# Performance work log

Measured on AMD Instinct MI355X. Metric: run time of the kernel, lower is better.

## Reference

```python
import jax, jax.numpy as jnp
import numpy as np
from jax import lax

K = 3  # kernel_size
PAD = K // 2

def setup_inputs() -> dict:
    key = jax.random.key(0)
    ks = jax.random.split(key, 8)
    B, C, H, W = 8, 96, 128, 128
    x = jax.random.normal(ks[0], (B, C, H, W), dtype=jnp.float32)
    s = 0.05
    dw_w = jax.random.normal(ks[1], (C, 1, 3, 3), dtype=jnp.float32) * s   # depthwise 3x3
    dw_b = jax.random.normal(ks[2], (C,), dtype=jnp.float32) * s
    pw1_w = jax.random.normal(ks[3], (C // 2, C), dtype=jnp.float32) * s   # 1x1: C -> C/2
    pw1_b = jax.random.normal(ks[4], (C // 2,), dtype=jnp.float32) * s
    pw2_w = jax.random.normal(ks[5], (K * K, C // 2), dtype=jnp.float32) * s  # 1x1: C/2 -> 9
    pw2_b = jax.random.normal(ks[6], (K * K,), dtype=jnp.float32) * s
    return {"x": x, "dw_w": dw_w, "dw_b": dw_b, "pw1_w": pw1_w,
            "pw1_b": pw1_b, "pw2_w": pw2_w, "pw2_b": pw2_b}

def _unfold3x3(x):
    # x: (B,C,H,W) -> patches (B,C,9,H,W), index order (di*3+dj) matching F.unfold
    B, C, H, W = x.shape
    xp = jnp.pad(x, ((0, 0), (0, 0), (PAD, PAD), (PAD, PAD)))
    return jnp.stack([xp[:, :, i:i + H, j:j + W] for i in range(K) for j in range(K)], axis=2)

def _forward(x, dw_w, dw_b, pw1_w, pw1_b, pw2_w, pw2_b):
    B, C, H, W = x.shape
    # kernel predictor: depthwise 3x3 -> 1x1 -> leaky_relu(0.2) -> 1x1
    h = lax.conv_general_dilated(x, dw_w, (1, 1), ((PAD, PAD), (PAD, PAD)),
                                 dimension_numbers=("NCHW", "OIHW", "NCHW"),
                                 feature_group_count=C)
    h = h + dw_b[None, :, None, None]
    h = jnp.einsum("bchw,oc->bohw", h, pw1_w) + pw1_b[None, :, None, None]
    h = jnp.where(h >= 0, h, 0.2 * h)  # LeakyReLU(0.2)
    kw = jnp.einsum("bchw,oc->bohw", h, pw2_w) + pw2_b[None, :, None, None]  # (B,9,H,W)
    kw = jax.nn.softmax(kw, axis=1)
    patches = _unfold3x3(x)                      # (B,C,9,H,W)
    x_smooth = jnp.einsum("bckhw,bkhw->bchw", patches, kw)
    return x_smooth

def reference(x, dw_w, dw_b, pw1_w, pw1_b, pw2_w, pw2_b):
    return _forward(x, dw_w, dw_b, pw1_w, pw1_b, pw2_w, pw2_b)
```

## Files before the change

kernel.cpp:

```cpp
#include <hip/hip_runtime.h>
#include <math.h>

#define Cc 96
#define Hh 128
#define Ww 128
#define HWsz (Hh*Ww)
#define TW 16
#define TH 8
#define LROW 18
#define LPLANE 180
#define CPAD 104

typedef _Float16 h2 __attribute__((ext_vector_type(2)));
typedef short    s8v __attribute__((ext_vector_type(8)));
typedef float    f4v __attribute__((ext_vector_type(4)));

__device__ __forceinline__ unsigned pkrtz_u(float a, float b) {
    return __builtin_bit_cast(unsigned, __builtin_amdgcn_cvt_pkrtz(a, b));
}
__device__ __forceinline__ h2 pk2(float a, float b) {
    return __builtin_bit_cast(h2, __builtin_amdgcn_cvt_pkrtz(a, b));
}
__device__ __forceinline__ h2 u2h(unsigned u) { return __builtin_bit_cast(h2, u); }
__device__ __forceinline__ unsigned cvt_pk_bf16(float lo, float hi) {
    unsigned r;
    asm("v_cvt_pk_bf16_f32 %0, %1, %2" : "=v"(r) : "v"(lo), "v"(hi));
    return r;
}

__host__ __device__ __forceinline__ unsigned f2bf(float f) {
    unsigned u = __float_as_uint(f);
    return (u + 0x7fffu + ((u >> 16) & 1u)) >> 16;
}

#define GETW(v, wi) ((wi)==0 ? (v).x : (wi)==1 ? (v).y : (wi)==2 ? (v).z : (v).w)

#define OFF_WDW 0
#define OFF_W2  480
#define OFF_P1B 704
#define OFF_A   768
#define NPK     3072
#define WLDS_N  752

__global__ void alpf_prep(const float* __restrict__ dw_w, const float* __restrict__ dw_b,
                          const float* __restrict__ pw1_w, const float* __restrict__ pw1_b,
                          const float* __restrict__ pw2_w, unsigned* __restrict__ wpk)
{
    int i = blockIdx.x * 256 + threadIdx.x;
    if (i >= NPK) return;
    unsigned v = 0u;
    if (i < OFF_W2) {
        int g = i / 120, rem = i % 120, ks = rem / 40, s = rem % 40;
        int chb = 32*ks + 8*g;
        if (s < 4) v = pkrtz_u(dw_b[chb + 2*s], dw_b[chb + 2*s + 1]);
        else { int t = (s - 4) / 4, d = (s - 4) % 4;
               v = pkrtz_u(dw_w[(chb + 2*d)*9 + t], dw_w[(chb + 2*d + 1)*9 + t]); }
    } else if (i < OFF_P1B) {
        int idx = i - OFF_W2; int g = idx / 56, s = idx % 56;
        if (s < 54) { int k = s / 6, mm = s % 6, m = mm / 2, rp = mm % 2;
            int o = 16*m + 4*g + 2*rp;
            v = pkrtz_u(pw2_w[k*48 + o], pw2_w[k*48 + o + 1]); }
    } else if (i < OFF_P1B + 48) {
        v = __float_as_uint(pw1_b[i - OFF_P1B]);
    } else if (i >= OFF_A) {
        int idx = i - OFF_A; int f = idx / 256, rem = idx % 256, l = rem / 4, d = rem % 4;
        int m = f / 3, ks = f % 3;
        int o  = 16*m + (l & 15);
        int ch = 32*ks + 8*(l >> 4) + 2*d;
        v = f2bf(pw1_w[o*Cc + ch]) | (f2bf(pw1_w[o*Cc + ch + 1]) << 16);
    }
    wpk[i] = v;
}

__global__ __launch_bounds__(256, 4)
void alpf_fused(const float* __restrict__ x,
                const float* __restrict__ pw2_b,
                const unsigned* __restrict__ wpk,
                float* __restrict__ out)
{
    __shared__ unsigned short lx[LPLANE * CPAD];
    __shared__ unsigned wlds[WLDS_N];

    const int tid = threadIdx.x;

    const int nwg   = gridDim.x;
    const int chunk = nwg >> 3;
    const int logical = (blockIdx.x & 7) * chunk + (blockIdx.x >> 3);
    const int tx = logical & 7;
    const int ty = (logical >> 3) & 15;
    const int b  = logical >> 7;
    const int x0 = tx * TW;
    const int y0 = ty * TH;
    const float* __restrict__ xb = x + (size_t)b * Cc * HWsz;

    if (tid < 188)
        *reinterpret_cast<uint4*>(&wlds[tid * 4]) =
            *reinterpret_cast<const uint4*>(wpk + tid * 4);

    const int lane = tid & 63;
    const int g    = lane >> 4;
    const int c15  = lane & 15;
    const int wv   = tid >> 6;

    s8v Af[9];
    #pragma unroll
    for (int f = 0; f < 9; ++f)
        Af[f] = __builtin_bit_cast(s8v,
            *reinterpret_cast<const uint4*>(wpk + OFF_A + (f*64 + lane)*4));

    for (int t = tid; t < 960; t += 256) {
        const int ri  = t / 96;
        const int rem = t - ri * 96;
        const int cp  = rem >> 1;
        const int ph  = rem & 1;
        const int gy  = y0 - 1 + ri;
        const bool okr = (gy >= 0) & (gy < Hh);
        const int gyc = okr ? gy : 0;
        const int chA = 2 * cp;
        const float* pA = xb + (size_t)chA * HWsz + gyc * Ww + x0 + 8 * ph;
        const float* pB = pA + HWsz;
        float4 a0 = *reinterpret_cast<const float4*>(pA);
        float4 a1 = *reinterpret_cast<const float4*>(pA + 4);
        float4 b0 = *reinterpret_cast<const float4*>(pB);
        float4 b1 = *reinterpret_cast<const float4*>(pB + 4);
        if (!okr) { a0 = make_float4(0,0,0,0); a1 = a0; b0 = a0; b1 = a0; }
        const int ecol  = ph ? (x0 + 16) : (x0 - 1);
        const bool oke  = okr & (ecol >= 0) & (ecol < Ww);
        const int ecolc = (ecol >= 0 && ecol < Ww) ? ecol : 0;
        const float* pE = xb + (size_t)chA * HWsz + gyc * Ww + ecolc;
        float ea = pE[0], eb = pE[HWsz];
        if (!oke) { ea = 0.f; eb = 0.f; }
        const int prow = ri * LROW + 1 + 8 * ph;
        #define STG(q, va, vb) \
            *reinterpret_cast<unsigned*>(&lx[(prow + (q)) * CPAD + chA]) = pkrtz_u(va, vb)
        STG(0, a0.x, b0.x); STG(1, a0.y, b0.y); STG(2, a0.z, b0.z); STG(3, a0.w, b0.w);
        STG(4, a1.x, b1.x); STG(5, a1.y, b1.y); STG(6, a1.z, b1.z); STG(7, a1.w, b1.w);
        #undef STG
        const int eq = ri * LROW + (ph ? 17 : 0);
        *reinterpret_cast<unsigned*>(&lx[eq * CPAD + chA]) = pkrtz_u(ea, eb);
    }
    __syncthreads();

    f4v acc[3][2];
    #pragma unroll
    for (int m = 0; m < 3; ++m) {
        const f4v bb = *reinterpret_cast<const f4v*>(&wlds[OFF_P1B + 16*m + 4*g]);
        acc[m][0] = bb;
        acc[m][1] = bb;
    }

    #pragma unroll
    for (int ks = 0; ks < 3; ++ks) {
        const int base = (g*3 + ks) * 40;
        const uint4 wb = *reinterpret_cast<const uint4*>(&wlds[base]);
        uint4 wt[9];
        #pragma unroll
        for (int t = 0; t < 9; ++t)
            wt[t] = *reinterpret_cast<const uint4*>(&wlds[base + 4 + 4*t]);
        uint4 xc_[4][3];
        #pragma unroll
        for (int r = 0; r < 4; ++r)
            #pragma unroll
            for (int d = 0; d < 3; ++d)
                xc_[r][d] = *reinterpret_cast<const uint4*>(
                    &lx[((2*wv + r)*LROW + c15 + d)*CPAD + 32*ks + 8*g]);
        #pragma unroll
        for (int n = 0; n < 2; ++n) {
            h2 b0 = u2h(wb.x), b1 = u2h(wb.y), b2 = u2h(wb.z), b3 = u2h(wb.w);
            #pragma unroll
            for (int t = 0; t < 9; ++t) {
                const int dy = t / 3, dx = t - 3*dy;
                const uint4 xv = xc_[n + dy][dx];
                b0 = __builtin_elementwise_fma(u2h(xv.x), u2h(wt[t].x), b0);
                b1 = __builtin_elementwise_fma(u2h(xv.y), u2h(wt[t].y), b1);
                b2 = __builtin_elementwise_fma(u2h(xv.z), u2h(wt[t].z), b2);
                b3 = __builtin_elementwise_fma(u2h(xv.w), u2h(wt[t].w), b3);
            }
            uint4 bq;
            bq.x = cvt_pk_bf16((float)b0.x, (float)b0.y);
            bq.y = cvt_pk_bf16((float)b1.x, (float)b1.y);
            bq.z = cvt_pk_bf16((float)b2.x, (float)b2.y);
            bq.w = cvt_pk_bf16((float)b3.x, (float)b3.y);
            const s8v Bf = __builtin_bit_cast(s8v, bq);
            acc[0][n] = __builtin_amdgcn_mfma_f32_16x16x32_bf16(Af[0 + ks], Bf, acc[0][n], 0, 0, 0);
            acc[1][n] = __builtin_amdgcn_mfma_f32_16x16x32_bf16(Af[3 + ks], Bf, acc[1][n], 0, 0, 0);
            acc[2][n] = __builtin_amdgcn_mfma_f32_16x16x32_bf16(Af[6 + ks], Bf, acc[2][n], 0, 0, 0);
        }
    }

    h2 tpk[2][3][2];
    #pragma unroll
    for (int n = 0; n < 2; ++n)
        #pragma unroll
        for (int m = 0; m < 3; ++m)
            #pragma unroll
            for (int rp = 0; rp < 2; ++rp) {
                float a = acc[m][n][2*rp], c = acc[m][n][2*rp + 1];
                a = (a >= 0.f) ? a : 0.2f * a;
                c = (c >= 0.f) ? c : 0.2f * c;
                tpk[n][m][rp] = pk2(a, c);
            }

    uint4 w2q[14];
    #pragma unroll
    for (int j = 0; j < 14; ++j)
        w2q[j] = *reinterpret_cast<const uint4*>(&wlds[OFF_W2 + g*56 + 4*j]);

    float kwr[2][9];
    #pragma unroll
    for (int k = 0; k < 9; ++k) {
        #pragma unroll
        for (int n = 0; n < 2; ++n) {
            h2 s = pk2(0.f, 0.f);
            #pragma unroll
            for (int m = 0; m < 3; ++m)
                #pragma unroll
                for (int rp = 0; rp < 2; ++rp) {
                    const int d = k*6 + 2*m + rp;
                    s = __builtin_elementwise_fma(tpk[n][m][rp],
                                                  u2h(GETW(w2q[d >> 2], d & 3)), s);
                }
            kwr[n][k] = (float)s.x + (float)s.y;
        }
    }
    #pragma unroll
    for (int n = 0; n < 2; ++n)
        #pragma unroll
        for (int k = 0; k < 9; ++k) {
            float v = kwr[n][k];
            v += __shfl_xor(v, 16);
            v += __shfl_xor(v, 32);
            kwr[n][k] = v + pw2_b[k];
        }

    const int nn  = (lane >> 4) & 1;
    const int chh = lane >> 5;
    const int row = 2*wv + nn;

    float kw[9];
    #pragma unroll
    for (int k = 0; k < 9; ++k) kw[k] = nn ? kwr[1][k] : kwr[0][k];

    float mx = kw[0];
    #pragma unroll
    for (int k = 1; k < 9; ++k) mx = fmaxf(mx, kw[k]);
    float sum = 0.f;
    #pragma unroll
    for (int k = 0; k < 9; ++k) { kw[k] = __expf(kw[k] - mx); sum += kw[k]; }
    const float inv = 1.f / sum;
    h2 kwp[9];
    #pragma unroll
    for (int k = 0; k < 9; ++k) { kw[k] *= inv; kwp[k] = pk2(kw[k], kw[k]); }

    const unsigned short* lb = &lx[(row * LROW + c15) * CPAD];
    float* __restrict__ ob = out + (size_t)b * Cc * HWsz + (size_t)(y0 + row) * Ww + (x0 + c15);
    #pragma unroll 2
    for (int cg = 0; cg < 6; ++cg) {
        const int c0 = chh * 48 + cg * 8;
        uint4 tp[9];
        #pragma unroll
        for (int k = 0; k < 9; ++k) {
            const int dy = k / 3, dx = k - 3 * dy;
            tp[k] = *reinterpret_cast<const uint4*>(&lb[(dy*LROW + dx)*CPAD + c0]);
        }
        #pragma unroll
        for (int l = 0; l < 4; ++l) {
            h2 a0 = u2h(GETW(tp[0], l)) * kwp[0];
            h2 a1 = u2h(GETW(tp[1], l)) * kwp[1];
            h2 a2 = u2h(GETW(tp[2], l)) * kwp[2];
            a0 = __builtin_elementwise_fma(u2h(GETW(tp[3], l)), kwp[3], a0);
            a1 = __builtin_elementwise_fma(u2h(GETW(tp[4], l)), kwp[4], a1);
            a2 = __builtin_elementwise_fma(u2h(GETW(tp[5], l)), kwp[5], a2);
            a0 = __builtin_elementwise_fma(u2h(GETW(tp[6], l)), kwp[6], a0);
            a1 = __builtin_elementwise_fma(u2h(GETW(tp[7], l)), kwp[7], a1);
            a2 = __builtin_elementwise_fma(u2h(GETW(tp[8], l)), kwp[8], a2);
            float olo = (float)a0.x + (float)a1.x + (float)a2.x;
            float ohi = (float)a0.y + (float)a1.y + (float)a2.y;
            ob[(size_t)(c0 + 2*l)     * HWsz] = olo;
            ob[(size_t)(c0 + 2*l + 1) * HWsz] = ohi;
        }
    }
}

extern "C" void kernel_launch(void* const* d_in, const int* in_sizes, int n_in,
                              void* d_out, int out_size, void* d_ws, size_t ws_size,
                              hipStream_t stream)
{
    const float* x     = (const float*)d_in[0];
    const float* dw_w  = (const float*)d_in[1];
    const float* dw_b  = (const float*)d_in[2];
    const float* pw1_w = (const float*)d_in[3];
    const float* pw1_b = (const float*)d_in[4];
    const float* pw2_w = (const float*)d_in[5];
    const float* pw2_b = (const float*)d_in[6];
    float* outp = (float*)d_out;
    unsigned* wpk = (unsigned*)d_ws;

    alpf_prep<<<(NPK + 255) / 256, 256, 0, stream>>>(dw_w, dw_b, pw1_w, pw1_b, pw2_w, wpk);

    const int B = in_sizes[0] / (Cc * HWsz);
    dim3 grid((Ww / TW) * (Hh / TH) * B);
    alpf_fused<<<grid, 256, 0, stream>>>(x, pw2_b, wpk, outp);
}
```

Measured before the change: 38.45 us.

## Pipeline input staging per 32-channel slice to overlap global loads with compute

The global-to-LDS staging of the input tile is split into three 32-channel slices. The next slice's global loads are issued into registers before the current slice's depthwise and MFMA work, and written to LDS afterwards with a barrier in between. This hides global load latency behind compute and lowers the upfront wait. LDS x reads now happen per tap inside the loop instead of being preloaded into a 4x3 register array, which changes register pressure and adds LDS reads. It also adds two extra barriers and keeps more registers live for the prefetch.

After: 63.47 us. +65.1%, slower.

```diff
diff --git a/kernel.cpp b/kernel.cpp
--- a/kernel.cpp
+++ b/kernel.cpp
@@ -108,28 +108,31 @@
         Af[f] = __builtin_bit_cast(s8v,
             *reinterpret_cast<const uint4*>(wpk + OFF_A + (f*64 + lane)*4));
 
-    for (int t = tid; t < 960; t += 256) {
-        const int ri  = t / 96;
-        const int rem = t - ri * 96;
-        const int cp  = rem >> 1;
-        const int ph  = rem & 1;
-        const int gy  = y0 - 1 + ri;
+    auto ldtask = [&](int u, int s, float4& a0, float4& a1, float4& b0, float4& b1,
+                      float& ea, float& eb) {
+        const int ri = u >> 5, rem = u & 31, cp = rem >> 1, ph = rem & 1;
+        const int gy = y0 - 1 + ri;
         const bool okr = (gy >= 0) & (gy < Hh);
         const int gyc = okr ? gy : 0;
-        const int chA = 2 * cp;
+        const int chA = 32*s + 2*cp;
         const float* pA = xb + (size_t)chA * HWsz + gyc * Ww + x0 + 8 * ph;
         const float* pB = pA + HWsz;
-        float4 a0 = *reinterpret_cast<const float4*>(pA);
-        float4 a1 = *reinterpret_cast<const float4*>(pA + 4);
-        float4 b0 = *reinterpret_cast<const float4*>(pB);
-        float4 b1 = *reinterpret_cast<const float4*>(pB + 4);
+        a0 = *reinterpret_cast<const float4*>(pA);
+        a1 = *reinterpret_cast<const float4*>(pA + 4);
+        b0 = *reinterpret_cast<const float4*>(pB);
+        b1 = *reinterpret_cast<const float4*>(pB + 4);
         if (!okr) { a0 = make_float4(0,0,0,0); a1 = a0; b0 = a0; b1 = a0; }
         const int ecol  = ph ? (x0 + 16) : (x0 - 1);
         const bool oke  = okr & (ecol >= 0) & (ecol < Ww);
         const int ecolc = (ecol >= 0 && ecol < Ww) ? ecol : 0;
         const float* pE = xb + (size_t)chA * HWsz + gyc * Ww + ecolc;
-        float ea = pE[0], eb = pE[HWsz];
+        ea = pE[0]; eb = pE[HWsz];
         if (!oke) { ea = 0.f; eb = 0.f; }
+    };
+    auto wrtask = [&](int u, int s, const float4& a0, const float4& a1,
+                      const float4& b0, const float4& b1, float ea, float eb) {
+        const int ri = u >> 5, rem = u & 31, cp = rem >> 1, ph = rem & 1;
+        const int chA = 32*s + 2*cp;
         const int prow = ri * LROW + 1 + 8 * ph;
         #define STG(q, va, vb) \
             *reinterpret_cast<unsigned*>(&lx[(prow + (q)) * CPAD + chA]) = pkrtz_u(va, vb)
@@ -138,10 +141,20 @@
         #undef STG
         const int eq = ri * LROW + (ph ? 17 : 0);
         *reinterpret_cast<unsigned*>(&lx[eq * CPAD + chA]) = pkrtz_u(ea, eb);
-    }
+    };
+
+    f4v acc[3][2];
+
+    float4 A0, A1, B0, B1; float EA, EB;
+    float4 C0, C1, D0, D1; float EC, ED;
+    const bool two = (tid < 64);
+
+    ldtask(tid, 0, A0, A1, B0, B1, EA, EB);
+    if (two) ldtask(tid + 256, 0, C0, C1, D0, D1, EC, ED);
+    wrtask(tid, 0, A0, A1, B0, B1, EA, EB);
+    if (two) wrtask(tid + 256, 0, C0, C1, D0, D1, EC, ED);
     __syncthreads();
 
-    f4v acc[3][2];
     #pragma unroll
     for (int m = 0; m < 3; ++m) {
         const f4v bb = *reinterpret_cast<const f4v*>(&wlds[OFF_P1B + 16*m + 4*g]);
@@ -151,40 +164,45 @@
 
     #pragma unroll
     for (int ks = 0; ks < 3; ++ks) {
-        const int base = (g*3 + ks) * 40;
-        const uint4 wb = *reinterpret_cast<const uint4*>(&wlds[base]);
-        uint4 wt[9];
-        #pragma unroll
-        for (int t = 0; t < 9; ++t)
-            wt[t] = *reinterpret_cast<const uint4*>(&wlds[base + 4 + 4*t]);
-        uint4 xc_[4][3];
-        #pragma unroll
-        for (int r = 0; r < 4; ++r)
+        if (ks < 2) {
+            ldtask(tid, ks + 1, A0, A1, B0, B1, EA, EB);
+            if (two) ldtask(tid + 256, ks + 1, C0, C1, D0, D1, EC, ED);
+        }
+        {
+            const int base = (g*3 + ks) * 40;
+            const uint4 wb = *reinterpret_cast<const uint4*>(&wlds[base]);
+            uint4 wt[9];
             #pragma unroll
-            for (int d = 0; d < 3; ++d)
-                xc_[r][d] = *reinterpret_cast<const uint4*>(
-                    &lx[((2*wv + r)*LROW + c15 + d)*CPAD + 32*ks + 8*g]);
-        #pragma unroll
-        for (int n = 0; n < 2; ++n) {
-            h2 b0 = u2h(wb.x), b1 = u2h(wb.y), b2 = u2h(wb.z), b3 = u2h(wb.w);
+            for (int t = 0; t < 9; ++t)
+                wt[t] = *reinterpret_cast<const uint4*>(&wlds[base + 4 + 4*t]);
             #pragma unroll
-            for (int t = 0; t < 9; ++t) {
-                const int dy = t / 3, dx = t - 3*dy;
-                const uint4 xv = xc_[n + dy][dx];
-                b0 = __builtin_elementwise_fma(u2h(xv.x), u2h(wt[t].x), b0);
-                b1 = __builtin_elementwise_fma(u2h(xv.y), u2h(wt[t].y), b1);
-                b2 = __builtin_elementwise_fma(u2h(xv.z), u2h(wt[t].z), b2);
-                b3 = __builtin_elementwise_fma(u2h(xv.w), u2h(wt[t].w), b3);
+            for (int n = 0; n < 2; ++n) {
+                h2 b0 = u2h(wb.x), b1 = u2h(wb.y), b2 = u2h(wb.z), b3 = u2h(wb.w);
+                #pragma unroll
+                for (int t = 0; t < 9; ++t) {
+                    const int dy = t / 3, dx = t - 3*dy;
+                    const uint4 xv = *reinterpret_cast<const uint4*>(
+                        &lx[((2*wv + n + dy)*LROW + c15 + dx)*CPAD + 32*ks + 8*g]);
+                    b0 = __builtin_elementwise_fma(u2h(xv.x), u2h(wt[t].x), b0);
+                    b1 = __builtin_elementwise_fma(u2h(xv.y), u2h(wt[t].y), b1);
+                    b2 = __builtin_elementwise_fma(u2h(xv.z), u2h(wt[t].z), b2);
+                    b3 = __builtin_elementwise_fma(u2h(xv.w), u2h(wt[t].w), b3);
+                }
+                uint4 bq;
+                bq.x = cvt_pk_bf16((float)b0.x, (float)b0.y);
+                bq.y = cvt_pk_bf16((float)b1.x, (float)b1.y);
+                bq.z = cvt_pk_bf16((float)b2.x, (float)b2.y);
+                bq.w = cvt_pk_bf16((float)b3.x, (float)b3.y);
+                const s8v Bf = __builtin_bit_cast(s8v, bq);
+                acc[0][n] = __builtin_amdgcn_mfma_f32_16x16x32_bf16(Af[0 + ks], Bf, acc[0][n], 0, 0, 0);
+                acc[1][n] = __builtin_amdgcn_mfma_f32_16x16x32_bf16(Af[3 + ks], Bf, acc[1][n], 0, 0, 0);
+                acc[2][n] = __builtin_amdgcn_mfma_f32_16x16x32_bf16(Af[6 + ks], Bf, acc[2][n], 0, 0, 0);
             }
-            uint4 bq;
-            bq.x = cvt_pk_bf16((float)b0.x, (float)b0.y);
-            bq.y = cvt_pk_bf16((float)b1.x, (float)b1.y);
-            bq.z = cvt_pk_bf16((float)b2.x, (float)b2.y);
-            bq.w = cvt_pk_bf16((float)b3.x, (float)b3.y);
-            const s8v Bf = __builtin_bit_cast(s8v, bq);
-            acc[0][n] = __builtin_amdgcn_mfma_f32_16x16x32_bf16(Af[0 + ks], Bf, acc[0][n], 0, 0, 0);
-            acc[1][n] = __builtin_amdgcn_mfma_f32_16x16x32_bf16(Af[3 + ks], Bf, acc[1][n], 0, 0, 0);
-            acc[2][n] = __builtin_amdgcn_mfma_f32_16x16x32_bf16(Af[6 + ks], Bf, acc[2][n], 0, 0, 0);
+        }
+        if (ks < 2) {
+            wrtask(tid, ks + 1, A0, A1, B0, B1, EA, EB);
+            if (two) wrtask(tid + 256, ks + 1, C0, C1, D0, D1, EC, ED);
+            __syncthreads();
         }
     }
 
```
